# Kernel optimization log

Measured on AMD Instinct MI355X. Metric: run time of the kernel, lower is better.

Reference implementation:

```python
import jax, jax.numpy as jnp
import numpy as np

B, S, C, L = 32, 256, 50, 20   # batch, max_seq_len, char_emb_dim, word_len
F, W = 30, 3                   # filter_num, char_window_size


def setup_inputs() -> dict:
    key = jax.random.key(0)
    k1, k2, k3 = jax.random.split(key, 3)
    char_embeddings_feature = jax.random.normal(k1, (B, S, C, L), dtype=jnp.float32)
    # torch grouped Conv1d weight: [out_ch=C*F, in_ch/groups=1, kernel=W]
    weight = jax.random.normal(k2, (C * F, 1, W), dtype=jnp.float32) * 0.1
    bias = jax.random.normal(k3, (C * F,), dtype=jnp.float32) * 0.1
    return {"char_embeddings_feature": char_embeddings_feature, "weight": weight, "bias": bias}


def reference(char_embeddings_feature, weight, bias):
    b, s, c, l = char_embeddings_feature.shape
    out_ch = weight.shape[0]
    # Fuse the per-position python loop: fold (batch, seq) into one conv batch dim.
    x = char_embeddings_feature.reshape(b * s, c, l)
    # Grouped (depthwise-style) conv: groups == c, each group has F output filters.
    y = jax.lax.conv_general_dilated(
        x, weight,
        window_strides=(1,), padding='VALID',
        dimension_numbers=('NCH', 'OIH', 'NCH'),
        feature_group_count=c,
    )  # [b*s, c*F, l-W+1]
    y = y + bias[None, :, None]
    # max-pool over conv output length, then restore (batch, seq)
    return y.max(axis=2).reshape(b, s, out_ch)
```

## Files before the change

kernel.cpp:

```cpp
#include <hip/hip_runtime.h>

constexpr int Bc = 32;
constexpr int Sc = 256;
constexpr int Cc = 50;
constexpr int Lc = 20;
constexpr int Fc = 30;
constexpr int Wc = 3;
constexpr int OUT_CH   = Cc * Fc;
constexpr int CONV_LEN = Lc - Wc + 1;
constexpr int XSZ      = Cc * Lc;
constexpr int BLOCK    = 256;
constexpr int CH_PER_T = 6;
constexpr int NP       = 4;

__global__ __launch_bounds__(BLOCK, 4)
void charcnn_kernel(const float* __restrict__ x,
                    const float* __restrict__ weight,
                    const float* __restrict__ bias,
                    float* __restrict__ out)
{
    __shared__ float xs[2][XSZ];

    const int t    = threadIdx.x;
    const int pos0 = blockIdx.x * NP;

    const bool stager = (t < XSZ / 4);
    const bool active = (t < OUT_CH / CH_PER_T);

    float w[CH_PER_T * Wc];
    float bb[CH_PER_T];
    if (active) {
        const float2* wp = (const float2*)(weight + t * (CH_PER_T * Wc));
        #pragma unroll
        for (int i = 0; i < (CH_PER_T * Wc) / 2; ++i) {
            const float2 q = wp[i];
            w[2*i] = q.x; w[2*i+1] = q.y;
        }
        const float2* bp = (const float2*)(bias + t * CH_PER_T);
        #pragma unroll
        for (int i = 0; i < CH_PER_T / 2; ++i) {
            const float2 q = bp[i];
            bb[2*i] = q.x; bb[2*i+1] = q.y;
        }
    }

    const int c = t / 5;

    if (stager)
        ((float4*)xs[0])[t] = ((const float4*)(x + (size_t)pos0 * XSZ))[t];

    for (int p = 0; p < NP; ++p) {
        const int buf = p & 1;

        float4 pre;
        const bool doPre = stager && (p + 1 < NP);
        if (doPre)
            pre = ((const float4*)(x + (size_t)(pos0 + p + 1) * XSZ))[t];

        __syncthreads();

        float res[CH_PER_T];
        if (active) {
            float v[Lc];
            const float4* rowv = (const float4*)(xs[buf] + c * Lc);
            #pragma unroll
            for (int i = 0; i < Lc / 4; ++i) {
                const float4 q = rowv[i];
                v[4*i+0] = q.x; v[4*i+1] = q.y; v[4*i+2] = q.z; v[4*i+3] = q.w;
            }

            #pragma unroll
            for (int j = 0; j < CH_PER_T; ++j) {
                const float w0 = w[3*j + 0];
                const float w1 = w[3*j + 1];
                const float w2 = w[3*j + 2];

                float cv[CONV_LEN];
                #pragma unroll
                for (int q = 0; q < CONV_LEN; ++q)
                    cv[q] = fmaf(v[q], w0, fmaf(v[q+1], w1, v[q+2] * w2));

                float m = fmaxf(fmaxf(cv[0], cv[1]), cv[2]);
                #pragma unroll
                for (int q = 3; q + 1 < CONV_LEN; q += 2)
                    m = fmaxf(fmaxf(m, cv[q]), cv[q+1]);
                m = fmaxf(m, cv[CONV_LEN - 1]);

                res[j] = m + bb[j];
            }
        }

        if (doPre)
            ((float4*)xs[buf ^ 1])[t] = pre;

        if (active) {
            float* op = out + (size_t)(pos0 + p) * OUT_CH + t * CH_PER_T;
            #pragma unroll
            for (int i = 0; i < CH_PER_T / 2; ++i)
                ((float2*)op)[i] = make_float2(res[2*i], res[2*i+1]);
        }
    }
}

extern "C" void kernel_launch(void* const* d_in, const int* in_sizes, int n_in,
                              void* d_out, int out_size, void* d_ws, size_t ws_size,
                              hipStream_t stream) {
    const float* x      = (const float*)d_in[0];
    const float* weight = (const float*)d_in[1];
    const float* bias   = (const float*)d_in[2];
    float* out          = (float*)d_out;

    const int nBlocks = (Bc * Sc) / NP;
    charcnn_kernel<<<nBlocks, BLOCK, 0, stream>>>(x, weight, bias, out);
}
```

Baseline: 28.05 us.

## Deepen global prefetch to two positions and use lightweight LDS-only barriers

Prefetches input rows two positions ahead in registers instead of one, fully unrolls the position loop, and replaces __syncthreads with a barrier that waits only on LDS counters so outstanding global loads are not drained at each sync. The conv/max loop is restructured to fold the max as it goes. The aim is to hide global load latency better. It relies on stager and active thread counts being equal (250), and the custom barrier depends on compiler ordering staying correct.

```diff
diff --git a/kernel.cpp b/kernel.cpp
--- a/kernel.cpp
+++ b/kernel.cpp
@@ -12,6 +12,13 @@
 constexpr int BLOCK    = 256;
 constexpr int CH_PER_T = 6;
 constexpr int NP       = 4;
+constexpr int ACT      = OUT_CH / CH_PER_T;
+
+static __device__ __forceinline__ void block_sync() {
+    asm volatile("s_waitcnt lgkmcnt(0)" ::: "memory");
+    __builtin_amdgcn_s_barrier();
+    asm volatile("" ::: "memory");
+}
 
 __global__ __launch_bounds__(BLOCK, 4)
 void charcnn_kernel(const float* __restrict__ x,
@@ -23,13 +30,11 @@
 
     const int t    = threadIdx.x;
     const int pos0 = blockIdx.x * NP;
-
-    const bool stager = (t < XSZ / 4);
-    const bool active = (t < OUT_CH / CH_PER_T);
+    const bool on  = (t < ACT);
 
     float w[CH_PER_T * Wc];
     float bb[CH_PER_T];
-    if (active) {
+    if (on) {
         const float2* wp = (const float2*)(weight + t * (CH_PER_T * Wc));
         #pragma unroll
         for (int i = 0; i < (CH_PER_T * Wc) / 2; ++i) {
@@ -46,21 +51,23 @@
 
     const int c = t / 5;
 
-    if (stager)
-        ((float4*)xs[0])[t] = ((const float4*)(x + (size_t)pos0 * XSZ))[t];
+    float4 preA, preB;
+    if (on) {
+        float4 s0 = ((const float4*)(x + (size_t)(pos0 + 0) * XSZ))[t];
+        preA      = ((const float4*)(x + (size_t)(pos0 + 1) * XSZ))[t];
+        ((float4*)xs[0])[t] = s0;
+    }
+    block_sync();
 
+    #pragma unroll
     for (int p = 0; p < NP; ++p) {
         const int buf = p & 1;
 
-        float4 pre;
-        const bool doPre = stager && (p + 1 < NP);
-        if (doPre)
-            pre = ((const float4*)(x + (size_t)(pos0 + p + 1) * XSZ))[t];
-
-        __syncthreads();
+        if (on && (p + 2 < NP))
+            preB = ((const float4*)(x + (size_t)(pos0 + p + 2) * XSZ))[t];
 
         float res[CH_PER_T];
-        if (active) {
+        if (on) {
             float v[Lc];
             const float4* rowv = (const float4*)(xs[buf] + c * Lc);
             #pragma unroll
@@ -75,30 +82,32 @@
                 const float w1 = w[3*j + 1];
                 const float w2 = w[3*j + 2];
 
-                float cv[CONV_LEN];
+                float m = fmaf(v[0], w0, fmaf(v[1], w1, v[2] * w2));
                 #pragma unroll
-                for (int q = 0; q < CONV_LEN; ++q)
-                    cv[q] = fmaf(v[q], w0, fmaf(v[q+1], w1, v[q+2] * w2));
-
-                float m = fmaxf(fmaxf(cv[0], cv[1]), cv[2]);
-                #pragma unroll
-                for (int q = 3; q + 1 < CONV_LEN; q += 2)
-                    m = fmaxf(fmaxf(m, cv[q]), cv[q+1]);
-                m = fmaxf(m, cv[CONV_LEN - 1]);
+                for (int q = 1; q + 1 < CONV_LEN; q += 2) {
+                    const float a = fmaf(v[q],   w0, fmaf(v[q+1], w1, v[q+2] * w2));
+                    const float b = fmaf(v[q+1], w0, fmaf(v[q+2], w1, v[q+3] * w2));
+                    m = fmaxf(fmaxf(m, a), b);
+                }
+                const float a = fmaf(v[CONV_LEN-1], w0,
+                                fmaf(v[CONV_LEN],   w1, v[CONV_LEN+1] * w2));
+                m = fmaxf(m, a);
 
                 res[j] = m + bb[j];
             }
-        }
 
-        if (doPre)
-            ((float4*)xs[buf ^ 1])[t] = pre;
+            if (p + 1 < NP)
+                ((float4*)xs[buf ^ 1])[t] = preA;
 
-        if (active) {
             float* op = out + (size_t)(pos0 + p) * OUT_CH + t * CH_PER_T;
             #pragma unroll
             for (int i = 0; i < CH_PER_T / 2; ++i)
                 ((float2*)op)[i] = make_float2(res[2*i], res[2*i+1]);
+
+            preA = preB;
         }
+
+        if (p + 1 < NP) block_sync();
     }
 }
 
```

New measurement: 29.27 us. 4.4% more time.
